# Kernel optimization log

Measured on AMD Instinct MI355X. Metric: run time of the kernel, lower is better.

## Reference

```python
import jax, jax.numpy as jnp
import numpy as np

H = 128
NH = 8
HD = H // NH  # 16
TANH_ALPHA = 10.0
LN_EPS = 1e-5


def _layer_norm(x, g, b):
    mu = jnp.mean(x, axis=-1, keepdims=True)
    var = jnp.mean((x - mu) ** 2, axis=-1, keepdims=True)
    return (x - mu) / jnp.sqrt(var + LN_EPS) * g + b


def setup_inputs() -> dict:
    key = jax.random.key(0)
    ks = jax.random.split(key, 24)
    B, N = 1024, 500

    def p(k, shape):
        return jax.random.normal(k, shape, dtype=jnp.float32) * 0.05

    inp = {
        "node_embeddings": jax.random.normal(ks[0], (B, N, H), jnp.float32),
        "graph_embeddings": jax.random.normal(ks[1], (B, H), jnp.float32),
        "first_node": jax.random.randint(ks[2], (B,), 0, N, jnp.int32),
        "current_node": jax.random.randint(ks[3], (B,), 0, N, jnp.int32),
        "mask": jax.random.randint(ks[4], (B, N), 0, 2, jnp.int32),
        # linear_first: Linear(384, 128)
        "W_first": p(ks[5], (H, 3 * H)),
        "b_first": p(ks[6], (H,)),
        # ln1 / ln2
        "g1": jnp.ones((H,), jnp.float32),
        "beta1": jnp.zeros((H,), jnp.float32),
        "g2": jnp.ones((H,), jnp.float32),
        "beta2": jnp.zeros((H,), jnp.float32),
        # LSTM(128,128) single layer, gate order i,f,g,o
        "W_ih": p(ks[7], (4 * H, H)),
        "W_hh": p(ks[8], (4 * H, H)),
        "b_ih": p(ks[9], (4 * H,)),
        "b_hh": p(ks[10], (4 * H,)),
        # attention / output projections (no bias)
        "Wq": p(ks[11], (H, H)),
        "Wk": p(ks[12], (H, H)),
        "Wv": p(ks[13], (H, H)),
        "Wproj": p(ks[14], (H, H)),
        # logitk: Linear(128,128) with bias
        "Wlk": p(ks[15], (H, H)),
        "blk": p(ks[16], (H,)),
    }
    return inp


def reference(node_embeddings, graph_embeddings, W_first, b_first, g1, beta1,
              W_ih, W_hh, b_ih, b_hh, g2, beta2, Wq, Wk, Wv, Wproj, Wlk, blk,
              first_node, current_node, mask):
    B, N, _ = node_embeddings.shape
    dt = node_embeddings.dtype

    # build_cache: K/V/logitK projections of all node embeddings
    ck = node_embeddings @ Wk.T                # [B,N,128]
    cv = node_embeddings @ Wv.T                # [B,N,128]
    lk = node_embeddings @ Wlk.T + blk         # [B,N,128]

    # context construction
    bidx = jnp.arange(B)
    first_emb = node_embeddings[bidx, first_node]    # [B,128]
    cur_emb = node_embeddings[bidx, current_node]    # [B,128]
    context = jnp.concatenate([graph_embeddings, first_emb, cur_emb], axis=1)
    context = _layer_norm(context @ W_first.T + b_first, g1, beta1)

    # single LSTM step from zero state (build_cache resets h,c to 0)
    gates = context @ W_ih.T + b_ih + b_hh           # h_prev = 0 -> no W_hh term
    i, f, g, o = jnp.split(gates, 4, axis=-1)
    c = jax.nn.sigmoid(i) * jnp.tanh(g)              # c_prev = 0
    h = jax.nn.sigmoid(o) * jnp.tanh(c)
    ctx = _layer_norm(h, g2, beta2)

    # multi-head single-query attention; note (e h) split: head is the FAST dim
    q = (ctx @ Wq.T).reshape(B, HD, NH).transpose(0, 2, 1)       # [B,h,e]
    k = ck.reshape(B, N, HD, NH).transpose(0, 3, 1, 2)           # [B,h,N,e]
    v = cv.reshape(B, N, HD, NH).transpose(0, 3, 1, 2)           # [B,h,N,e]
    maskf = mask.astype(dt)
    scores = jnp.einsum('bhe,bhne->bhn', q, k) / np.sqrt(HD) + maskf[:, None, :]
    att = jax.nn.softmax(scores, axis=-1)
    oh = jnp.einsum('bhn,bhne->bhe', att, v)                     # [B,h,e]
    att_out = oh.reshape(B, H)                                   # (h e): h slow, e fast

    context_emb = att_out @ Wproj.T                              # [B,128]
    comp = jnp.einsum('be,bne->bn', lk, context_emb[:, None, :].squeeze(1)[:, :][None].squeeze(0) if False else context_emb) if False else jnp.einsum('bne,be->bn', lk, context_emb)
    comp = comp / np.sqrt(H)
    comp = TANH_ALPHA * jnp.tanh(comp)
    out = jnp.where(mask == 1, -jnp.inf, comp)
    return out
```

## Files before the change

### kernel.cpp

```cpp
#include <hip/hip_runtime.h>
#include <math.h>

#define NBATCH 1024
#define NNODE  500
#define HDIM   128
#define NHEAD  8
#define G1K    4
#define SPLIT  2
#define CPB    4
#define CHUNK  64
#define PSTRIDE 1056
#define RSQRT_H 0.08838834764831845f
#define MASK_NEG (-1e30f)

__device__ __forceinline__ float wave_sum64(float v) {
    #pragma unroll
    for (int off = 32; off >= 1; off >>= 1) v += __shfl_xor(v, off, 64);
    return v;
}
__device__ __forceinline__ float wave_max64(float v) {
    #pragma unroll
    for (int off = 32; off >= 1; off >>= 1) v = fmaxf(v, __shfl_xor(v, off, 64));
    return v;
}

__device__ __forceinline__ void gload_lds16(const float* g, float4* l) {
    __builtin_amdgcn_global_load_lds(
        (const __attribute__((address_space(1))) unsigned int*)g,
        (__attribute__((address_space(3))) unsigned int*)l, 16, 0, 0);
}

template<int G>
__device__ __forceinline__ void block_ln(float (&x)[G], const float* __restrict__ gw,
                                         const float* __restrict__ bw,
                                         int t, int lane, int wv, float (*wpart)[G])
{
    float s[G];
    #pragma unroll
    for (int g = 0; g < G; ++g) s[g] = x[g];
    #pragma unroll
    for (int off = 32; off >= 1; off >>= 1) {
        #pragma unroll
        for (int g = 0; g < G; ++g) s[g] += __shfl_xor(s[g], off, 64);
    }
    if (lane == 0) {
        #pragma unroll
        for (int g = 0; g < G; ++g) wpart[wv][g] = s[g];
    }
    __syncthreads();
    float mu[G];
    #pragma unroll
    for (int g = 0; g < G; ++g) mu[g] = (wpart[0][g] + wpart[1][g]) * (1.f/128.f);
    __syncthreads();
    #pragma unroll
    for (int g = 0; g < G; ++g) { float d = x[g] - mu[g]; s[g] = d * d; }
    #pragma unroll
    for (int off = 32; off >= 1; off >>= 1) {
        #pragma unroll
        for (int g = 0; g < G; ++g) s[g] += __shfl_xor(s[g], off, 64);
    }
    if (lane == 0) {
        #pragma unroll
        for (int g = 0; g < G; ++g) wpart[wv][g] = s[g];
    }
    __syncthreads();
    float gv = gw[t], bv = bw[t];
    #pragma unroll
    for (int g = 0; g < G; ++g) {
        float var = (wpart[0][g] + wpart[1][g]) * (1.f/128.f);
        x[g] = (x[g] - mu[g]) / sqrtf(var + 1e-5f) * gv + bv;
    }
    __syncthreads();
}

__global__ __launch_bounds__(128) void k1_context(
    const float* __restrict__ node, const float* __restrict__ graph,
    const int* __restrict__ firstn, const int* __restrict__ curn,
    const float* __restrict__ W_first, const float* __restrict__ b_first,
    const float* __restrict__ g1, const float* __restrict__ beta1,
    const float* __restrict__ W_ih, const float* __restrict__ b_ih,
    const float* __restrict__ b_hh, const float* __restrict__ g2,
    const float* __restrict__ beta2, const float* __restrict__ Wq,
    const float* __restrict__ Wk, float* __restrict__ qW_out)
{
    const int t = threadIdx.x;
    const int lane = t & 63, wv = t >> 6;
    const int b0 = blockIdx.x * G1K;
    __shared__ float ctx[G1K][384];
    __shared__ float bufB[G1K][128];
    __shared__ float wpart[2][G1K];

    #pragma unroll
    for (int g = 0; g < G1K; ++g) {
        int b = b0 + g;
        ctx[g][t]       = graph[b*HDIM + t];
        ctx[g][128 + t] = node[((size_t)b*NNODE + firstn[b])*HDIM + t];
        ctx[g][256 + t] = node[((size_t)b*NNODE + curn[b])*HDIM + t];
    }
    __syncthreads();

    float x[G1K];
    {
        float bf = b_first[t];
        #pragma unroll
        for (int g = 0; g < G1K; ++g) x[g] = bf;
        for (int j = 0; j < 384; ++j) {
            float w = W_first[t*384 + j];
            #pragma unroll
            for (int g = 0; g < G1K; ++g) x[g] += ctx[g][j] * w;
        }
    }
    block_ln<G1K>(x, g1, beta1, t, lane, wv, wpart);

    #pragma unroll
    for (int g = 0; g < G1K; ++g) bufB[g][t] = x[g];
    __syncthreads();

    float gi[G1K], gg[G1K], go[G1K];
    {
        float bi = b_ih[t]       + b_hh[t];
        float bg = b_ih[256 + t] + b_hh[256 + t];
        float bo = b_ih[384 + t] + b_hh[384 + t];
        #pragma unroll
        for (int g = 0; g < G1K; ++g) { gi[g] = bi; gg[g] = bg; go[g] = bo; }
        for (int j = 0; j < 128; ++j) {
            float wi = W_ih[(size_t)t*128 + j];
            float wg = W_ih[(size_t)(256 + t)*128 + j];
            float wo = W_ih[(size_t)(384 + t)*128 + j];
            #pragma unroll
            for (int g = 0; g < G1K; ++g) {
                float v = bufB[g][j];
                gi[g] += v * wi; gg[g] += v * wg; go[g] += v * wo;
            }
        }
    }
    #pragma unroll
    for (int g = 0; g < G1K; ++g) {
        float ig = 1.f / (1.f + expf(-gi[g]));
        float cc = ig * tanhf(gg[g]);
        float og = 1.f / (1.f + expf(-go[g]));
        x[g] = og * tanhf(cc);
    }
    block_ln<G1K>(x, g2, beta2, t, lane, wv, wpart);

    #pragma unroll
    for (int g = 0; g < G1K; ++g) bufB[g][t] = x[g];
    __syncthreads();

    float q8[G1K];
    #pragma unroll
    for (int g = 0; g < G1K; ++g) q8[g] = 0.f;
    for (int j = 0; j < 128; ++j) {
        float w = Wq[t*128 + j];
        #pragma unroll
        for (int g = 0; g < G1K; ++g) q8[g] += bufB[g][j] * w;
    }
    __syncthreads();
    #pragma unroll
    for (int g = 0; g < G1K; ++g) bufB[g][t] = q8[g];
    __syncthreads();

    for (int h = 0; h < NHEAD; ++h) {
        float a[G1K];
        #pragma unroll
        for (int g = 0; g < G1K; ++g) a[g] = 0.f;
        for (int e = 0; e < 16; ++e) {
            float w = Wk[(e*8 + h)*HDIM + t];
            #pragma unroll
            for (int g = 0; g < G1K; ++g) a[g] += bufB[g][e*8 + h] * w;
        }
        #pragma unroll
        for (int g = 0; g < G1K; ++g)
            qW_out[((size_t)(b0 + g)*NHEAD + h)*HDIM + t] = 0.25f * a[g];
    }
}

__global__ __launch_bounds__(256) void k2a_pipe(
    const float* __restrict__ node, const int* __restrict__ mask,
    const float* __restrict__ qW, float* __restrict__ part)
{
    const int b = blockIdx.x >> 1;
    const int s = blockIdx.x & (SPLIT - 1);
    const int tid = threadIdx.x;
    const int lane = tid & 63;
    const int wave = tid >> 6;
    const int nbase = s * (CPB * CHUNK);

    __shared__ float4 bufs[2][CHUNK*32];
    __shared__ __align__(16) float s_qw[NHEAD*HDIM];
    __shared__ float  s_p[NHEAD*CHUNK];
    __shared__ float  s_m[NHEAD], s_l[NHEAD], s_c[NHEAD];

    const float* nodeb = node + (size_t)b*NNODE*HDIM;

    auto stage = [&](float4* buf, int ck) {
        const int base = nbase + ck*CHUNK;
        #pragma unroll
        for (int i = 0; i < 8; ++i) {
            int slot = i*256 + tid;
            int r = slot >> 5, qp = slot & 31;
            int gn = base + r;
            if (gn < NNODE) {
                const float* g = nodeb + (size_t)gn*HDIM + ((qp ^ (r & 31)) << 2);
                gload_lds16(g, &buf[slot]);
            }
        }
        int nval = NNODE - base;
        if (nval < CHUNK) {
            for (int slot = tid; slot < CHUNK*32; slot += 256)
                if ((slot >> 5) >= nval) buf[slot] = make_float4(0.f,0.f,0.f,0.f);
        }
    };

    stage(bufs[0], 0);
    ((float4*)s_qw)[tid] = ((const float4*)(qW + (size_t)b*NHEAD*HDIM))[tid];
    if (tid < NHEAD) { s_m[tid] = -INFINITY; s_l[tid] = 0.f; }

    float4 acc[NHEAD];
    #pragma unroll
    for (int h = 0; h < NHEAD; ++h) acc[h] = make_float4(0.f, 0.f, 0.f, 0.f);

    const int sn = tid & 63;
    const int hp = tid >> 6;
    const int sg = tid >> 5;
    const int aq = tid & 31;

    __syncthreads();

    for (int ck = 0; ck < CPB; ++ck) {
        float4* A = bufs[ck & 1];
        if (ck + 1 < CPB) stage(bufs[(ck + 1) & 1], ck + 1);
        const int base = nbase + ck*CHUNK;

        {
            float s0 = 0.f, s1 = 0.f;
            const int rb = sn*32, sw = sn & 31;
            const float4* qa = (const float4*)(s_qw + hp*HDIM);
            const float4* qb = (const float4*)(s_qw + (hp + 4)*HDIM);
            #pragma unroll 8
            for (int qq = 0; qq < 32; ++qq) {
                float4 nv = A[rb + (qq ^ sw)];
                float4 av = qa[qq];
                float4 bv = qb[qq];
                s0 += nv.x*av.x + nv.y*av.y + nv.z*av.z + nv.w*av.w;
                s1 += nv.x*bv.x + nv.y*bv.y + nv.z*bv.z + nv.w*bv.w;
            }
            int gn = base + sn;
            if (gn < NNODE) {
                float mf = (float)mask[(size_t)b*NNODE + gn];
                s0 += mf; s1 += mf;
            } else { s0 = -INFINITY; s1 = -INFINITY; }
            s_p[hp*64 + sn] = s0;
            s_p[(hp + 4)*64 + sn] = s1;
        }
        __syncthreads();

        for (int hh = wave; hh < NHEAD; hh += 4) {
            float sv = s_p[hh*64 + lane];
            float mx = wave_max64(sv);
            float mO = s_m[hh];
            float mN = fmaxf(mO, mx);
            float pv = __expf(sv - mN);
            s_p[hh*64 + lane] = pv;
            float sm = wave_sum64(pv);
            if (lane == 0) {
                float corr = __expf(mO - mN);
                s_c[hh] = corr;
                s_l[hh] = s_l[hh]*corr + sm;
                s_m[hh] = mN;
            }
        }
        __syncthreads();

        {
            #pragma unroll
            for (int h = 0; h < NHEAD; ++h) {
                float c = s_c[h];
                acc[h].x *= c; acc[h].y *= c; acc[h].z *= c; acc[h].w *= c;
            }
            #pragma unroll
            for (int j = 0; j < 8; ++j) {
                int n = sg*8 + j;
                float4 nv = A[n*32 + (aq ^ (n & 31))];
                #pragma unroll
                for (int h = 0; h < NHEAD; ++h) {
                    float p = s_p[h*64 + n];
                    acc[h].x += p*nv.x; acc[h].y += p*nv.y;
                    acc[h].z += p*nv.z; acc[h].w += p*nv.w;
                }
            }
        }
        __syncthreads();
    }

    float* pbase = part + (size_t)blockIdx.x * PSTRIDE;
    #pragma unroll
    for (int h = 0; h < NHEAD; ++h) bufs[0][(sg*8 + h)*32 + aq] = acc[h];
    if (tid < NHEAD) { pbase[tid] = s_m[tid]; pbase[8 + tid] = s_l[tid]; }
    __syncthreads();
    {
        const int h2 = tid >> 5, q2 = tid & 31;
        float4 tot = make_float4(0.f, 0.f, 0.f, 0.f);
        #pragma unroll
        for (int ss = 0; ss < 8; ++ss) {
            float4 v = bufs[0][(ss*8 + h2)*32 + q2];
            tot.x += v.x; tot.y += v.y; tot.z += v.z; tot.w += v.w;
        }
        *(float4*)(pbase + 16 + h2*HDIM + q2*4) = tot;
    }
}

__global__ __launch_bounds__(256) void k2b_reduce(
    const float* __restrict__ part, const float* __restrict__ Wv,
    const float* __restrict__ Wproj, const float* __restrict__ Wlk,
    const float* __restrict__ blk, float* __restrict__ wce_out,
    float* __restrict__ bias_out)
{
    const int b = blockIdx.x;
    const int tid = threadIdx.x;
    __shared__ __align__(16) float s_an[NHEAD*HDIM];
    __shared__ float s_ao[HDIM], s_ce[HDIM];

    {
        const int h = tid >> 5, q = tid & 31;
        const float* pb = part + (size_t)b*SPLIT*PSTRIDE;
        float m[SPLIT], l[SPLIT];
        float gm = -INFINITY;
        #pragma unroll
        for (int s = 0; s < SPLIT; ++s) {
            m[s] = pb[s*PSTRIDE + h];
            l[s] = pb[s*PSTRIDE + 8 + h];
            gm = fmaxf(gm, m[s]);
        }
        float lsum = 0.f;
        float4 tot = make_float4(0.f, 0.f, 0.f, 0.f);
        #pragma unroll
        for (int s = 0; s < SPLIT; ++s) {
            float f = __expf(m[s] - gm);
            lsum += l[s] * f;
            float4 v = *(const float4*)(pb + s*PSTRIDE + 16 + h*HDIM + q*4);
            tot.x += f*v.x; tot.y += f*v.y; tot.z += f*v.z; tot.w += f*v.w;
        }
        float inv = 1.f / lsum;
        tot.x *= inv; tot.y *= inv; tot.z *= inv; tot.w *= inv;
        *(float4*)(s_an + h*HDIM + q*4) = tot;
    }
    __syncthreads();

    if (tid < HDIM) {
        const int c = tid, h = c >> 4, e = c & 15;
        const int row = e*8 + h;
        float oh = 0.f;
        for (int d = 0; d < HDIM; ++d) oh += s_an[h*HDIM + d] * Wv[row*HDIM + d];
        s_ao[c] = oh;
    }
    __syncthreads();
    if (tid < HDIM) {
        const int c = tid;
        float ce = 0.f;
        for (int j = 0; j < HDIM; ++j) ce += s_ao[j] * Wproj[c*HDIM + j];
        s_ce[c] = ce;
    }
    __syncthreads();
    if (tid < HDIM) {
        const int d = tid;
        float w = 0.f;
        for (int c = 0; c < HDIM; ++c) w += s_ce[c] * Wlk[c*HDIM + d];
        wce_out[(size_t)b*HDIM + d] = w * RSQRT_H;
        if (d == 0) {
            float bb = 0.f;
            for (int c = 0; c < HDIM; ++c) bb += s_ce[c] * blk[c];
            bias_out[b] = bb * RSQRT_H;
        }
    }
}

__global__ __launch_bounds__(256) void k2_flash_mono(
    const float* __restrict__ node, const int* __restrict__ mask,
    const float* __restrict__ qW, const float* __restrict__ Wv,
    const float* __restrict__ Wproj, const float* __restrict__ Wlk,
    const float* __restrict__ blk, float* __restrict__ wce_out,
    float* __restrict__ bias_out)
{
    const int b = blockIdx.x;
    const int tid = threadIdx.x;
    const int lane = tid & 63;
    const int wave = tid >> 6;

    __shared__ float4 s_tile[64*32];
    __shared__ __align__(16) float s_qw[NHEAD*HDIM];
    __shared__ float  s_p[NHEAD*64];
    __shared__ float  s_m[NHEAD], s_l[NHEAD], s_c[NHEAD];
    __shared__ float  s_ao[HDIM], s_ce[HDIM];

    ((float4*)s_qw)[tid] = ((const float4*)(qW + (size_t)b*NHEAD*HDIM))[tid];
    if (tid < NHEAD) { s_m[tid] = -INFINITY; s_l[tid] = 0.f; }

    float4 acc[NHEAD];
    #pragma unroll
    for (int h = 0; h < NHEAD; ++h) acc[h] = make_float4(0.f, 0.f, 0.f, 0.f);

    const int sn = tid & 63;
    const int hp = tid >> 6;
    const int sg = tid >> 5;
    const int aq = tid & 31;
    const float* nodeb = node + (size_t)b*NNODE*HDIM;

    for (int tile = 0; tile < 8; ++tile) {
        const int base = tile*64;
        #pragma unroll
        for (int i = 0; i < 8; ++i) {
            int idx = i*256 + tid;
            int r = idx >> 5, qq = idx & 31;
            int gn = base + r;
            float4 v = make_float4(0.f, 0.f, 0.f, 0.f);
            if (gn < NNODE) v = *(const float4*)(nodeb + (size_t)gn*HDIM + qq*4);
            s_tile[r*32 + (qq ^ (r & 31))] = v;
        }
        __syncthreads();
        {
            float s0 = 0.f, s1 = 0.f;
            const int rb = sn*32, sw = sn & 31;
            const float4* qa = (const float4*)(s_qw + hp*HDIM);
            const float4* qb = (const float4*)(s_qw + (hp + 4)*HDIM);
            #pragma unroll 8
            for (int qq = 0; qq < 32; ++qq) {
                float4 nv = s_tile[rb + (qq ^ sw)];
                float4 av = qa[qq];
                float4 bv = qb[qq];
                s0 += nv.x*av.x + nv.y*av.y + nv.z*av.z + nv.w*av.w;
                s1 += nv.x*bv.x + nv.y*bv.y + nv.z*bv.z + nv.w*bv.w;
            }
            int gn = base + sn;
            if (gn < NNODE) {
                float mf = (float)mask[(size_t)b*NNODE + gn];
                s0 += mf; s1 += mf;
            } else { s0 = -INFINITY; s1 = -INFINITY; }
            s_p[hp*64 + sn] = s0;
            s_p[(hp + 4)*64 + sn] = s1;
        }
        __syncthreads();
        for (int hh = wave; hh < NHEAD; hh += 4) {
            float sv = s_p[hh*64 + lane];
            float mx = wave_max64(sv);
            float mO = s_m[hh];
            float mN = fmaxf(mO, mx);
            float pv = __expf(sv - mN);
            s_p[hh*64 + lane] = pv;
            float sm = wave_sum64(pv);
            if (lane == 0) {
                float corr = __expf(mO - mN);
                s_c[hh] = corr;
                s_l[hh] = s_l[hh]*corr + sm;
                s_m[hh] = mN;
            }
        }
        __syncthreads();
        {
            #pragma unroll
            for (int h = 0; h < NHEAD; ++h) {
                float c = s_c[h];
                acc[h].x *= c; acc[h].y *= c; acc[h].z *= c; acc[h].w *= c;
            }
            #pragma unroll
            for (int j = 0; j < 8; ++j) {
                int n = sg*8 + j;
                float4 nv = s_tile[n*32 + (aq ^ (n & 31))];
                #pragma unroll
                for (int h = 0; h < NHEAD; ++h) {
                    float p = s_p[h*64 + n];
                    acc[h].x += p*nv.x; acc[h].y += p*nv.y;
                    acc[h].z += p*nv.z; acc[h].w += p*nv.w;
                }
            }
        }
        __syncthreads();
    }
    #pragma unroll
    for (int h = 0; h < NHEAD; ++h) s_tile[(sg*8 + h)*32 + aq] = acc[h];
    __syncthreads();
    {
        const int h2 = tid >> 5, q2 = tid & 31;
        float4 tot = make_float4(0.f, 0.f, 0.f, 0.f);
        #pragma unroll
        for (int s = 0; s < 8; ++s) {
            float4 v = s_tile[(s*8 + h2)*32 + q2];
            tot.x += v.x; tot.y += v.y; tot.z += v.z; tot.w += v.w;
        }
        float inv = 1.f / s_l[h2];
        tot.x *= inv; tot.y *= inv; tot.z *= inv; tot.w *= inv;
        ((float4*)s_qw)[h2*32 + q2] = tot;
    }
    __syncthreads();
    if (tid < HDIM) {
        const int c = tid, h = c >> 4, e = c & 15;
        const int row = e*8 + h;
        float oh = 0.f;
        for (int d = 0; d < HDIM; ++d) oh += s_qw[h*HDIM + d] * Wv[row*HDIM + d];
        s_ao[c] = oh;
    }
    __syncthreads();
    if (tid < HDIM) {
        const int c = tid;
        float ce = 0.f;
        for (int j = 0; j < HDIM; ++j) ce += s_ao[j] * Wproj[c*HDIM + j];
        s_ce[c] = ce;
    }
    __syncthreads();
    if (tid < HDIM) {
        const int d = tid;
        float w = 0.f;
        for (int c = 0; c < HDIM; ++c) w += s_ce[c] * Wlk[c*HDIM + d];
        wce_out[(size_t)b*HDIM + d] = w * RSQRT_H;
        if (d == 0) {
            float bb = 0.f;
            for (int c = 0; c < HDIM; ++c) bb += s_ce[c] * blk[c];
            bias_out[b] = bb * RSQRT_H;
        }
    }
}

__global__ __launch_bounds__(256) void k3_out(
    const float* __restrict__ node, const int* __restrict__ mask,
    const float* __restrict__ wce, const float* __restrict__ biasv,
    float* __restrict__ out)
{
    const int slot = (int)((blockIdx.x*256u + threadIdx.x) >> 5);
    const int q = threadIdx.x & 31;
    const int b = slot / NNODE;
    const float4 nv = *(const float4*)(node + (size_t)slot*HDIM + q*4);
    const float4 wv = *(const float4*)(wce + (size_t)b*HDIM + q*4);
    float p = nv.x*wv.x + nv.y*wv.y + nv.z*wv.z + nv.w*wv.w;
    #pragma unroll
    for (int off = 16; off >= 1; off >>= 1) p += __shfl_xor(p, off, 32);
    if (q == 0) {
        float v = 10.f * tanhf(p + biasv[b]);
        out[slot] = (mask[slot] == 1) ? MASK_NEG : v;
    }
}

extern "C" void kernel_launch(void* const* d_in, const int* in_sizes, int n_in,
                              void* d_out, int out_size, void* d_ws, size_t ws_size,
                              hipStream_t stream) {
    const float* node    = (const float*)d_in[0];
    const float* graph   = (const float*)d_in[1];
    const int*   firstn  = (const int*)d_in[2];
    const int*   curn    = (const int*)d_in[3];
    const int*   mask    = (const int*)d_in[4];
    const float* W_first = (const float*)d_in[5];
    const float* b_first = (const float*)d_in[6];
    const float* g1      = (const float*)d_in[7];
    const float* beta1   = (const float*)d_in[8];
    const float* g2      = (const float*)d_in[9];
    const float* beta2   = (const float*)d_in[10];
    const float* W_ih    = (const float*)d_in[11];
    const float* b_ih    = (const float*)d_in[13];
    const float* b_hh    = (const float*)d_in[14];
    const float* Wq      = (const float*)d_in[15];
    const float* Wk      = (const float*)d_in[16];
    const float* Wv      = (const float*)d_in[17];
    const float* Wproj   = (const float*)d_in[18];
    const float* Wlk     = (const float*)d_in[19];
    const float* blk     = (const float*)d_in[20];
    float* out = (float*)d_out;

    float* qW    = (float*)d_ws;
    float* wce   = qW + (size_t)NBATCH*NHEAD*HDIM;
    float* biasv = wce + (size_t)NBATCH*HDIM;
    float* part  = biasv + NBATCH;
    const size_t need = ((size_t)NBATCH*NHEAD*HDIM + (size_t)NBATCH*HDIM + NBATCH
                         + (size_t)NBATCH*SPLIT*PSTRIDE) * sizeof(float);

    k1_context<<<NBATCH/G1K, 128, 0, stream>>>(node, graph, firstn, curn,
        W_first, b_first, g1, beta1, W_ih, b_ih, b_hh, g2, beta2, Wq, Wk, qW);
    if (ws_size >= need) {
        k2a_pipe<<<NBATCH*SPLIT, 256, 0, stream>>>(node, mask, qW, part);
        k2b_reduce<<<NBATCH, 256, 0, stream>>>(part, Wv, Wproj, Wlk, blk,
            wce, biasv);
    } else {
        k2_flash_mono<<<NBATCH, 256, 0, stream>>>(node, mask, qW, Wv, Wproj,
            Wlk, blk, wce, biasv);
    }
    k3_out<<<(NBATCH*NNODE)/8, 256, 0, stream>>>(node, mask, wce, biasv, out);
}
```

Measured before the change: 213.8 us.

## Register-staged node prefetch in attention kernel and vectorize context GEMVs

Replaces the double-buffered global-to-LDS async load pipeline in the attention pass with a register-prefetch scheme. Each thread loads a quarter-row of the next chunk into registers, computes scores from registers with shuffle reductions, then writes the tile to a single LDS buffer. This halves LDS use and overlaps the next chunk's global loads with the PV accumulation. The context kernel now uses float4 weight and LDS loads and processes 2 batches per block instead of 4, trading more weight re-reads for more blocks. Register pressure rises from holding 8 float4 values plus the 8 accumulators.

```diff
diff --git a/kernel.cpp b/kernel.cpp
--- a/kernel.cpp
+++ b/kernel.cpp
@@ -5,7 +5,7 @@
 #define NNODE  500
 #define HDIM   128
 #define NHEAD  8
-#define G1K    4
+#define G1K    2
 #define SPLIT  2
 #define CPB    4
 #define CHUNK  64
@@ -22,12 +22,6 @@
     #pragma unroll
     for (int off = 32; off >= 1; off >>= 1) v = fmaxf(v, __shfl_xor(v, off, 64));
     return v;
-}
-
-__device__ __forceinline__ void gload_lds16(const float* g, float4* l) {
-    __builtin_amdgcn_global_load_lds(
-        (const __attribute__((address_space(1))) unsigned int*)g,
-        (__attribute__((address_space(3))) unsigned int*)l, 16, 0, 0);
 }
 
 template<int G>
@@ -86,8 +80,8 @@
     const int t = threadIdx.x;
     const int lane = t & 63, wv = t >> 6;
     const int b0 = blockIdx.x * G1K;
-    __shared__ float ctx[G1K][384];
-    __shared__ float bufB[G1K][128];
+    __shared__ __align__(16) float ctx[G1K][384];
+    __shared__ __align__(16) float bufB[G1K][128];
     __shared__ float wpart[2][G1K];
 
     #pragma unroll
@@ -101,13 +95,17 @@
 
     float x[G1K];
     {
+        const float4* Wf4 = (const float4*)W_first;
         float bf = b_first[t];
         #pragma unroll
         for (int g = 0; g < G1K; ++g) x[g] = bf;
-        for (int j = 0; j < 384; ++j) {
-            float w = W_first[t*384 + j];
-            #pragma unroll
-            for (int g = 0; g < G1K; ++g) x[g] += ctx[g][j] * w;
+        for (int j4 = 0; j4 < 96; ++j4) {
+            float4 w = Wf4[t*96 + j4];
+            #pragma unroll
+            for (int g = 0; g < G1K; ++g) {
+                float4 c = ((const float4*)ctx[g])[j4];
+                x[g] += c.x*w.x + c.y*w.y + c.z*w.z + c.w*w.w;
+            }
         }
     }
     block_ln<G1K>(x, g1, beta1, t, lane, wv, wpart);
@@ -118,19 +116,22 @@
 
     float gi[G1K], gg[G1K], go[G1K];
     {
+        const float4* Wih4 = (const float4*)W_ih;
         float bi = b_ih[t]       + b_hh[t];
         float bg = b_ih[256 + t] + b_hh[256 + t];
         float bo = b_ih[384 + t] + b_hh[384 + t];
         #pragma unroll
         for (int g = 0; g < G1K; ++g) { gi[g] = bi; gg[g] = bg; go[g] = bo; }
-        for (int j = 0; j < 128; ++j) {
-            float wi = W_ih[(size_t)t*128 + j];
-            float wg = W_ih[(size_t)(256 + t)*128 + j];
-            float wo = W_ih[(size_t)(384 + t)*128 + j];
+        for (int j4 = 0; j4 < 32; ++j4) {
+            float4 wi = Wih4[(size_t)t*32 + j4];
+            float4 wg = Wih4[(size_t)(256 + t)*32 + j4];
+            float4 wo = Wih4[(size_t)(384 + t)*32 + j4];
             #pragma unroll
             for (int g = 0; g < G1K; ++g) {
-                float v = bufB[g][j];
-                gi[g] += v * wi; gg[g] += v * wg; go[g] += v * wo;
+                float4 v = ((const float4*)bufB[g])[j4];
+                gi[g] += v.x*wi.x + v.y*wi.y + v.z*wi.z + v.w*wi.w;
+                gg[g] += v.x*wg.x + v.y*wg.y + v.z*wg.z + v.w*wg.w;
+                go[g] += v.x*wo.x + v.y*wo.y + v.z*wo.z + v.w*wo.w;
             }
         }
     }
@@ -150,10 +151,16 @@
     float q8[G1K];
     #pragma unroll
     for (int g = 0; g < G1K; ++g) q8[g] = 0.f;
-    for (int j = 0; j < 128; ++j) {
-        float w = Wq[t*128 + j];
-        #pragma unroll
-        for (int g = 0; g < G1K; ++g) q8[g] += bufB[g][j] * w;
+    {
+        const float4* Wq4 = (const float4*)Wq;
+        for (int j4 = 0; j4 < 32; ++j4) {
+            float4 w = Wq4[t*32 + j4];
+            #pragma unroll
+            for (int g = 0; g < G1K; ++g) {
+                float4 v = ((const float4*)bufB[g])[j4];
+                q8[g] += v.x*w.x + v.y*w.y + v.z*w.z + v.w*w.w;
+            }
+        }
     }
     __syncthreads();
     #pragma unroll
@@ -175,83 +182,90 @@
     }
 }
 
-__global__ __launch_bounds__(256) void k2a_pipe(
+__global__ __launch_bounds__(256) void k2a_reg(
     const float* __restrict__ node, const int* __restrict__ mask,
     const float* __restrict__ qW, float* __restrict__ part)
 {
-    const int b = blockIdx.x >> 1;
-    const int s = blockIdx.x & (SPLIT - 1);
+    const int b   = blockIdx.x >> 1;
+    const int s   = blockIdx.x & (SPLIT - 1);
     const int tid = threadIdx.x;
     const int lane = tid & 63;
     const int wave = tid >> 6;
     const int nbase = s * (CPB * CHUNK);
 
-    __shared__ float4 bufs[2][CHUNK*32];
-    __shared__ __align__(16) float s_qw[NHEAD*HDIM];
-    __shared__ float  s_p[NHEAD*CHUNK];
-    __shared__ float  s_m[NHEAD], s_l[NHEAD], s_c[NHEAD];
-
-    const float* nodeb = node + (size_t)b*NNODE*HDIM;
-
-    auto stage = [&](float4* buf, int ck) {
-        const int base = nbase + ck*CHUNK;
-        #pragma unroll
-        for (int i = 0; i < 8; ++i) {
-            int slot = i*256 + tid;
-            int r = slot >> 5, qp = slot & 31;
-            int gn = base + r;
-            if (gn < NNODE) {
-                const float* g = nodeb + (size_t)gn*HDIM + ((qp ^ (r & 31)) << 2);
-                gload_lds16(g, &buf[slot]);
-            }
-        }
-        int nval = NNODE - base;
-        if (nval < CHUNK) {
-            for (int slot = tid; slot < CHUNK*32; slot += 256)
-                if ((slot >> 5) >= nval) buf[slot] = make_float4(0.f,0.f,0.f,0.f);
-        }
-    };
-
-    stage(bufs[0], 0);
-    ((float4*)s_qw)[tid] = ((const float4*)(qW + (size_t)b*NHEAD*HDIM))[tid];
-    if (tid < NHEAD) { s_m[tid] = -INFINITY; s_l[tid] = 0.f; }
-
-    float4 acc[NHEAD];
-    #pragma unroll
-    for (int h = 0; h < NHEAD; ++h) acc[h] = make_float4(0.f, 0.f, 0.f, 0.f);
-
-    const int sn = tid & 63;
-    const int hp = tid >> 6;
+    const int rn = tid >> 2;
+    const int dq = tid & 3;
     const int sg = tid >> 5;
     const int aq = tid & 31;
 
+    __shared__ __align__(16) float4 s_tile[CHUNK*32];
+    __shared__ __align__(16) float  s_qw[NHEAD*HDIM];
+    __shared__ float s_p[NHEAD*CHUNK];
+    __shared__ float s_mask[CHUNK];
+    __shared__ float s_m[NHEAD], s_l[NHEAD], s_c[NHEAD];
+
+    const float* nodeb = node + (size_t)b*NNODE*HDIM;
+    const int*   maskb = mask + (size_t)b*NNODE;
+
+    float4 R[8];
+    {
+        int gn = nbase + rn;
+        if (gn < NNODE) {
+            const float4* src = (const float4*)(nodeb + (size_t)gn*HDIM) + dq*8;
+            #pragma unroll
+            for (int k = 0; k < 8; ++k) R[k] = src[k];
+        } else {
+            #pragma unroll
+            for (int k = 0; k < 8; ++k) R[k] = make_float4(0.f,0.f,0.f,0.f);
+        }
+    }
+    ((float4*)s_qw)[tid] = ((const float4*)(qW + (size_t)b*NHEAD*HDIM))[tid];
+    if (tid < CHUNK) {
+        int gn = nbase + tid;
+        s_mask[tid] = (gn < NNODE) ? (float)maskb[gn] : 0.f;
+    }
+    if (tid < NHEAD) { s_m[tid] = -INFINITY; s_l[tid] = 0.f; }
+
+    float4 acc[NHEAD];
+    #pragma unroll
+    for (int h = 0; h < NHEAD; ++h) acc[h] = make_float4(0.f,0.f,0.f,0.f);
+
     __syncthreads();
 
     for (int ck = 0; ck < CPB; ++ck) {
-        float4* A = bufs[ck & 1];
-        if (ck + 1 < CPB) stage(bufs[(ck + 1) & 1], ck + 1);
         const int base = nbase + ck*CHUNK;
 
         {
-            float s0 = 0.f, s1 = 0.f;
-            const int rb = sn*32, sw = sn & 31;
-            const float4* qa = (const float4*)(s_qw + hp*HDIM);
-            const float4* qb = (const float4*)(s_qw + (hp + 4)*HDIM);
-            #pragma unroll 8
-            for (int qq = 0; qq < 32; ++qq) {
-                float4 nv = A[rb + (qq ^ sw)];
-                float4 av = qa[qq];
-                float4 bv = qb[qq];
-                s0 += nv.x*av.x + nv.y*av.y + nv.z*av.z + nv.w*av.w;
-                s1 += nv.x*bv.x + nv.y*bv.y + nv.z*bv.z + nv.w*bv.w;
-            }
-            int gn = base + sn;
-            if (gn < NNODE) {
-                float mf = (float)mask[(size_t)b*NNODE + gn];
-                s0 += mf; s1 += mf;
-            } else { s0 = -INFINITY; s1 = -INFINITY; }
-            s_p[hp*64 + sn] = s0;
-            s_p[(hp + 4)*64 + sn] = s1;
+            float sc[NHEAD];
+            #pragma unroll
+            for (int h = 0; h < NHEAD; ++h) {
+                const float4* qh = (const float4*)(s_qw + h*HDIM) + dq*8;
+                float t0 = 0.f;
+                #pragma unroll
+                for (int k = 0; k < 8; ++k) {
+                    float4 w = qh[k];
+                    t0 += R[k].x*w.x + R[k].y*w.y + R[k].z*w.z + R[k].w*w.w;
+                }
+                sc[h] = t0;
+            }
+            #pragma unroll
+            for (int h = 0; h < NHEAD; ++h) {
+                sc[h] += __shfl_xor(sc[h], 1, 64);
+                sc[h] += __shfl_xor(sc[h], 2, 64);
+            }
+            if (dq == 0) {
+                int gn = base + rn;
+                float mf = s_mask[rn];
+                bool oob = (gn >= NNODE);
+                #pragma unroll
+                for (int h = 0; h < NHEAD; ++h)
+                    s_p[h*64 + rn] = oob ? -INFINITY : sc[h] + mf;
+            }
+        }
+        #pragma unroll
+        for (int k = 0; k < 8; ++k) {
+            int q = dq*8 + k;
+            s_tile[rn*32 + (q ^ (rn & 31))] = R[k];
         }
         __syncthreads();
 
@@ -272,6 +286,22 @@
         }
         __syncthreads();
 
+        if (ck + 1 < CPB) {
+            int gn = base + CHUNK + rn;
+            if (gn < NNODE) {
+                const float4* src = (const float4*)(nodeb + (size_t)gn*HDIM) + dq*8;
+                #pragma unroll
+                for (int k = 0; k < 8; ++k) R[k] = src[k];
+            } else {
+                #pragma unroll
+                for (int k = 0; k < 8; ++k) R[k] = make_float4(0.f,0.f,0.f,0.f);
+            }
+            if (tid < CHUNK) {
+                int gm = base + CHUNK + tid;
+                s_mask[tid] = (gm < NNODE) ? (float)maskb[gm] : 0.f;
+            }
+        }
+
         {
             #pragma unroll
             for (int h = 0; h < NHEAD; ++h) {
@@ -281,7 +311,7 @@
             #pragma unroll
             for (int j = 0; j < 8; ++j) {
                 int n = sg*8 + j;
-                float4 nv = A[n*32 + (aq ^ (n & 31))];
+                float4 nv = s_tile[n*32 + (aq ^ (n & 31))];
                 #pragma unroll
                 for (int h = 0; h < NHEAD; ++h) {
                     float p = s_p[h*64 + n];
@@ -295,15 +325,15 @@
 
     float* pbase = part + (size_t)blockIdx.x * PSTRIDE;
     #pragma unroll
-    for (int h = 0; h < NHEAD; ++h) bufs[0][(sg*8 + h)*32 + aq] = acc[h];
+    for (int h = 0; h < NHEAD; ++h) s_tile[(sg*8 + h)*32 + aq] = acc[h];
     if (tid < NHEAD) { pbase[tid] = s_m[tid]; pbase[8 + tid] = s_l[tid]; }
     __syncthreads();
     {
         const int h2 = tid >> 5, q2 = tid & 31;
-        float4 tot = make_float4(0.f, 0.f, 0.f, 0.f);
+        float4 tot = make_float4(0.f,0.f,0.f,0.f);
         #pragma unroll
         for (int ss = 0; ss < 8; ++ss) {
-            float4 v = bufs[0][(ss*8 + h2)*32 + q2];
+            float4 v = s_tile[(ss*8 + h2)*32 + q2];
             tot.x += v.x; tot.y += v.y; tot.z += v.z; tot.w += v.w;
         }
         *(float4*)(pbase + 16 + h2*HDIM + q2*4) = tot;
@@ -333,7 +363,7 @@
             gm = fmaxf(gm, m[s]);
         }
         float lsum = 0.f;
-        float4 tot = make_float4(0.f, 0.f, 0.f, 0.f);
+        float4 tot = make_float4(0.f,0.f,0.f,0.f);
         #pragma unroll
         for (int s = 0; s < SPLIT; ++s) {
             float f = __expf(m[s] - gm);
@@ -398,7 +428,7 @@
 
     float4 acc[NHEAD];
     #pragma unroll
-    for (int h = 0; h < NHEAD; ++h) acc[h] = make_float4(0.f, 0.f, 0.f, 0.f);
+    for (int h = 0; h < NHEAD; ++h) acc[h] = make_float4(0.f,0.f,0.f,0.f);
 
     const int sn = tid & 63;
     const int hp = tid >> 6;
@@ -413,7 +443,7 @@
             int idx = i*256 + tid;
             int r = idx >> 5, qq = idx & 31;
             int gn = base + r;
-            float4 v = make_float4(0.f, 0.f, 0.f, 0.f);
+            float4 v = make_float4(0.f,0.f,0.f,0.f);
             if (gn < NNODE) v = *(const float4*)(nodeb + (size_t)gn*HDIM + qq*4);
             s_tile[r*32 + (qq ^ (r & 31))] = v;
         }
@@ -481,7 +511,7 @@
     __syncthreads();
     {
         const int h2 = tid >> 5, q2 = tid & 31;
-        float4 tot = make_float4(0.f, 0.f, 0.f, 0.f);
+        float4 tot = make_float4(0.f,0.f,0.f,0.f);
         #pragma unroll
         for (int s = 0; s < 8; ++s) {
             float4 v = s_tile[(s*8 + h2)*32 + q2];
@@ -574,7 +604,7 @@
     k1_context<<<NBATCH/G1K, 128, 0, stream>>>(node, graph, firstn, curn,
         W_first, b_first, g1, beta1, W_ih, b_ih, b_hh, g2, beta2, Wq, Wk, qW);
     if (ws_size >= need) {
-        k2a_pipe<<<NBATCH*SPLIT, 256, 0, stream>>>(node, mask, qW, part);
+        k2a_reg<<<NBATCH*SPLIT, 256, 0, stream>>>(node, mask, qW, part);
         k2b_reduce<<<NBATCH, 256, 0, stream>>>(part, Wv, Wproj, Wlk, blk,
             wce, biasv);
     } else {
```

New measurement: 230.6 us. +7.9%, slower.
